# Performance work log

Hardware: AMD Instinct MI355X
Metric: run time of the kernel (lower is better)

The kernel has to match this reference:

```python
import jax, jax.numpy as jnp
import numpy as np

B, N, D_IN, D_OUT = 4, 2048, 1024, 1024


def setup_inputs() -> dict:
    key = jax.random.key(0)
    kx, kq, kk, kv = jax.random.split(key, 4)
    x = jax.random.normal(kx, (B, N, D_IN), dtype=jnp.float32)
    # torch Linear(d_in, d_out, bias=False): y = x @ W.T, W ~ U(-1/sqrt(d_in), 1/sqrt(d_in)).
    # Store as [d_in, d_out] so y = x @ W.
    bound = 1.0 / np.sqrt(D_IN)
    Wq = jax.random.uniform(kq, (D_IN, D_OUT), jnp.float32, -bound, bound)
    Wk = jax.random.uniform(kk, (D_IN, D_OUT), jnp.float32, -bound, bound)
    Wv = jax.random.uniform(kv, (D_IN, D_OUT), jnp.float32, -bound, bound)
    return {"x": x, "Wq": Wq, "Wk": Wk, "Wv": Wv}


def reference(x, Wq, Wk, Wv):
    # x: [B, N, d_in]
    q = jnp.einsum("bnd,de->bne", x, Wq)  # [B, N, d_out]
    k = jnp.einsum("bnd,de->bne", x, Wk)
    v = jnp.einsum("bnd,de->bne", x, Wv)
    n = x.shape[1]
    scores = jnp.einsum("bqe,bke->bqk", q, k)  # [B, N, N]
    causal = jnp.triu(jnp.ones((n, n), dtype=bool), k=1)  # True above diagonal -> masked
    scores = jnp.where(causal, -jnp.inf, scores)
    scale = 1.0 / jnp.sqrt(jnp.asarray(k.shape[-1], dtype=scores.dtype))
    weights = jax.nn.softmax(scores * scale, axis=-1)
    # dropout with drop_rate=0.0 is identity
    return jnp.einsum("bqk,bke->bqe", weights, v)  # [B, N, d_out]
```

## Files before the change

### kernel.cpp

```cpp
#include <hip/hip_runtime.h>

typedef float  f4v  __attribute__((ext_vector_type(4)));
typedef short  s8v  __attribute__((ext_vector_type(8)));

__device__ __forceinline__ ushort f2b(float f) {
    union { float f; unsigned int u; } v; v.f = f;
    unsigned int u = v.u;
    u += 0x7fffu + ((u >> 16) & 1u);
    return (ushort)(u >> 16);
}
__device__ __forceinline__ float b2f(ushort u) {
    union { unsigned int u; float f; } v; v.u = ((unsigned int)u) << 16;
    return v.f;
}

__device__ __forceinline__ void async16(const ushort* g, ushort* ldsp) {
    __builtin_amdgcn_global_load_lds(
        (const __attribute__((address_space(1))) unsigned int*)g,
        (__attribute__((address_space(3))) unsigned int*)ldsp, 16, 0, 0);
}

__global__ __launch_bounds__(256) void cast_f32_bf16(const float* __restrict__ in,
                                                     ushort* __restrict__ out,
                                                     float* __restrict__ l, int n4) {
    int i = blockIdx.x * 256 + threadIdx.x;
    if (i < 8192) l[i] = 0.f;
    if (i < n4) {
        float4 f = ((const float4*)in)[i];
        ushort4 o;
        o.x = f2b(f.x); o.y = f2b(f.y); o.z = f2b(f.z); o.w = f2b(f.w);
        ((ushort4*)out)[i] = o;
    }
}

__global__ __launch_bounds__(256) void transpose_cast(const float* __restrict__ w0,
                                                      const float* __restrict__ w1,
                                                      const float* __restrict__ w2,
                                                      ushort* __restrict__ out) {
    __shared__ float tile[32][33];
    const float* W = (blockIdx.z == 0) ? w0 : (blockIdx.z == 1 ? w1 : w2);
    ushort* O = out + (size_t)blockIdx.z * (1024u * 1024u);
    int x0 = blockIdx.x * 32, y0 = blockIdx.y * 32;
    int tx = threadIdx.x, ty = threadIdx.y;
    for (int i = 0; i < 4; i++)
        tile[ty + i * 8][tx] = W[(size_t)(y0 + ty + i * 8) * 1024 + x0 + tx];
    __syncthreads();
    for (int i = 0; i < 4; i++)
        O[(size_t)(x0 + ty + i * 8) * 1024 + y0 + tx] = f2b(tile[tx][ty + i * 8]);
}


#define RD_A4(buf_)                                                                   \
    _Pragma("unroll") for (int mi = 0; mi < 4; mi++)                                  \
    _Pragma("unroll") for (int s = 0; s < 2; s++)                                     \
        af[mi][s] = *(const s8v*)&(buf_)[(wm + mi * 16 + l16) * 64 +                  \
                                         (((s * 4 + quad) ^ (l16 & 7)) * 8)];

#define RD_B2(buf_, NI0_)                                                             \
    _Pragma("unroll") for (int j = 0; j < 2; j++)                                     \
    _Pragma("unroll") for (int s = 0; s < 2; s++)                                     \
        bf[j][s] = *(const s8v*)&(buf_)[(wn + ((NI0_) + j) * 16 + l16) * 64 +         \
                                        (((s * 4 + quad) ^ (l16 & 7)) * 8)];

#define MFMA16(NI0_)                                                                  \
    _Pragma("unroll") for (int mi = 0; mi < 4; mi++)                                  \
    _Pragma("unroll") for (int j = 0; j < 2; j++)                                     \
    _Pragma("unroll") for (int s = 0; s < 2; s++)                                     \
        acc[mi][(NI0_) + j] = __builtin_amdgcn_mfma_f32_16x16x32_bf16(                \
            af[mi][s], bf[j][s], acc[mi][(NI0_) + j], 0, 0, 0);

__global__ __launch_bounds__(512, 2) void gemm_qkv(const ushort* __restrict__ A,
                                                   const ushort* __restrict__ Wt,
                                                   ushort* __restrict__ q,
                                                   ushort* __restrict__ k,
                                                   ushort* __restrict__ vt) {
    constexpr int K = 1024;
    extern __shared__ ushort lds[];

    const int L = blockIdx.x;
    const int xcd = L & 7, idx = L >> 3;
    const int ci = xcd >> 1, cj = xcd & 1;
    const int mo = idx >> 3, no = idx & 7;
    const int m0 = (ci * 8 + mo) * 256;
    const int n0 = (cj * 8 + no) * 192;

    const int tid = threadIdx.x;
    const int w = tid >> 6, lane = tid & 63, quad = lane >> 4, l16 = lane & 15;
    const int wm = (w >> 1) * 64, wn = (w & 1) * 96;

    ushort* a0 = lds;
    ushort* a1 = lds + 16384;
    ushort* a2 = lds + 32768;
    ushort* b0 = lds + 49152;
    ushort* b1 = lds + 61440;

    const int lr = lane >> 3;
    const int lc8 = (lane & 7) ^ lr;
    const ushort* Ab = A  + (size_t)(m0 + w * 8 + lr) * K + lc8 * 8;
    const ushort* Bb = Wt + (size_t)(n0 + w * 8 + lr) * K + lc8 * 8;
    const int dW = w * 512;

#define ISSUE_A(buf_, kk_, a_) async16(Ab + (size_t)(a_) * 64 * K + (kk_), (buf_) + (a_) * 4096 + dW)
#define ISSUE_B(buf_, kk_, c_) async16(Bb + (size_t)(c_) * 64 * K + (kk_), (buf_) + (c_) * 4096 + dW)

    f4v acc[4][6];
    #pragma unroll
    for (int mi = 0; mi < 4; mi++)
        #pragma unroll
        for (int ni = 0; ni < 6; ni++) acc[mi][ni] = 0;

    #pragma unroll
    for (int a = 0; a < 4; a++) ISSUE_A(a0, 0, a);
    #pragma unroll
    for (int c = 0; c < 3; c++) ISSUE_B(b0, 0, c);
    #pragma unroll
    for (int a = 0; a < 4; a++) ISSUE_A(a1, 64, a);
    asm volatile("s_waitcnt vmcnt(4)" ::: "memory");
    asm volatile("s_barrier" ::: "memory");

    for (int t = 0; t < 16; ++t) {
        const int kB = (t + 1) * 64;
        const int kA = (t + 2) * 64;
        s8v af[4][2], bf[2][2];

        RD_A4(a0)
        RD_B2(b0, 0)
        if (t < 15) {
            ISSUE_B(b1, kB, 0);
            ISSUE_B(b1, kB, 1);
            ISSUE_B(b1, kB, 2);
        }
        asm volatile("s_barrier" ::: "memory");
        __builtin_amdgcn_s_setprio(1);
        MFMA16(0)
        __builtin_amdgcn_s_setprio(0);
        asm volatile("s_barrier" ::: "memory");

        RD_B2(b0, 2)
        if (t < 14) {
            ISSUE_A(a2, kA, 0);
            ISSUE_A(a2, kA, 1);
        }
        asm volatile("s_barrier" ::: "memory");
        __builtin_amdgcn_s_setprio(1);
        MFMA16(2)
        __builtin_amdgcn_s_setprio(0);
        asm volatile("s_barrier" ::: "memory");

        RD_B2(b0, 4)
        if (t < 14) {
            ISSUE_A(a2, kA, 2);
            ISSUE_A(a2, kA, 3);
        }
        asm volatile("s_barrier" ::: "memory");
        __builtin_amdgcn_s_setprio(1);
        MFMA16(4)
        __builtin_amdgcn_s_setprio(0);

        if (t < 14)       asm volatile("s_waitcnt vmcnt(4)" ::: "memory");
        else if (t == 14) asm volatile("s_waitcnt vmcnt(0)" ::: "memory");
        asm volatile("s_barrier" ::: "memory");

        ushort* ta = a0; a0 = a1; a1 = a2; a2 = ta;
        ushort* tb = b0; b0 = b1; b1 = tb;
    }

    #pragma unroll
    for (int mi = 0; mi < 4; mi++)
        #pragma unroll
        for (int ni = 0; ni < 6; ni++) {
            int row = m0 + wm + mi * 16 + quad * 4;
            int col = n0 + wn + ni * 16 + l16;
            int z = col >> 10, cz = col & 1023;
            f4v v = acc[mi][ni];
            if (z < 2) {
                ushort* C = (z == 0) ? q : k;
                #pragma unroll
                for (int rr = 0; rr < 4; rr++)
                    C[(size_t)(row + rr) * 1024 + cz] = f2b(v[rr]);
            } else {
                int b = row >> 11, tok = row & 2047;
                ushort4 pk;
                pk.x = f2b(v[0]); pk.y = f2b(v[1]); pk.z = f2b(v[2]); pk.w = f2b(v[3]);
                *(ushort4*)&vt[(size_t)b * (1024u * 2048u) + (size_t)cz * 2048 + tok] = pk;
            }
        }
#undef ISSUE_A
#undef ISSUE_B
}

__global__ __launch_bounds__(512, 2) void sgemm_qk(const ushort* __restrict__ Q,
                                                   const ushort* __restrict__ Km,
                                                   ushort* __restrict__ E,
                                                   float* __restrict__ l) {
    constexpr int K = 1024;
    extern __shared__ ushort lds[];

    const int L = blockIdx.x;
    const int xcd = L & 7, i = L >> 3;
    const int t = (xcd < 4) ? (xcd * 26 + i) : (104 + (xcd - 4) * 25 + i);
    const int b = t / 51;
    int tt = t - b * 51;
    int mt = 0;
    for (;; mt++) {
        int c = (4 * (mt + 1) + 2) / 3;
        if (tt < c) break;
        tt -= c;
    }
    const int nt = tt;
    const int m0 = mt * 256, n0 = nt * 192;
    const ushort* A  = Q  + (size_t)b * 2048 * 1024;
    const ushort* Bt = Km + (size_t)b * 2048 * 1024;
    ushort* Cb = E + (size_t)b * 2048 * 2048;
    float* lb = l + (size_t)b * 2048;

    const int tid = threadIdx.x;
    const int w = tid >> 6, lane = tid & 63, quad = lane >> 4, l16 = lane & 15;
    const int wm = (w >> 1) * 64, wn = (w & 1) * 96;

    ushort* a0 = lds;
    ushort* a1 = lds + 16384;
    ushort* a2 = lds + 32768;
    ushort* b0 = lds + 49152;
    ushort* b1 = lds + 61440;

    const int lr = lane >> 3;
    const int lc8 = (lane & 7) ^ lr;
    const ushort* Ab = A  + (size_t)(m0 + w * 8 + lr) * K + lc8 * 8;
    const ushort* Bb = Bt + (size_t)(n0 + w * 8 + lr) * K + lc8 * 8;
    const int dW = w * 512;

#define ISSUE_A(buf_, kk_, a_) async16(Ab + (size_t)(a_) * 64 * K + (kk_), (buf_) + (a_) * 4096 + dW)
#define ISSUE_B(buf_, kk_, c_) async16(Bb + (size_t)(c_) * 64 * K + (kk_), (buf_) + (c_) * 4096 + dW)

    f4v acc[4][6];
    #pragma unroll
    for (int mi = 0; mi < 4; mi++)
        #pragma unroll
        for (int ni = 0; ni < 6; ni++) acc[mi][ni] = 0;

    #pragma unroll
    for (int a = 0; a < 4; a++) ISSUE_A(a0, 0, a);
    #pragma unroll
    for (int c = 0; c < 3; c++) ISSUE_B(b0, 0, c);
    #pragma unroll
    for (int a = 0; a < 4; a++) ISSUE_A(a1, 64, a);
    asm volatile("s_waitcnt vmcnt(4)" ::: "memory");
    asm volatile("s_barrier" ::: "memory");

    for (int tk = 0; tk < 16; ++tk) {
        const int kB = (tk + 1) * 64;
        const int kA = (tk + 2) * 64;
        s8v af[4][2], bf[2][2];

        RD_A4(a0)
        RD_B2(b0, 0)
        if (tk < 15) {
            ISSUE_B(b1, kB, 0);
            ISSUE_B(b1, kB, 1);
            ISSUE_B(b1, kB, 2);
        }
        asm volatile("s_barrier" ::: "memory");
        __builtin_amdgcn_s_setprio(1);
        MFMA16(0)
        __builtin_amdgcn_s_setprio(0);
        asm volatile("s_barrier" ::: "memory");

        RD_B2(b0, 2)
        if (tk < 14) {
            ISSUE_A(a2, kA, 0);
            ISSUE_A(a2, kA, 1);
        }
        asm volatile("s_barrier" ::: "memory");
        __builtin_amdgcn_s_setprio(1);
        MFMA16(2)
        __builtin_amdgcn_s_setprio(0);
        asm volatile("s_barrier" ::: "memory");

        RD_B2(b0, 4)
        if (tk < 14) {
            ISSUE_A(a2, kA, 2);
            ISSUE_A(a2, kA, 3);
        }
        asm volatile("s_barrier" ::: "memory");
        __builtin_amdgcn_s_setprio(1);
        MFMA16(4)
        __builtin_amdgcn_s_setprio(0);

        if (tk < 14)       asm volatile("s_waitcnt vmcnt(4)" ::: "memory");
        else if (tk == 14) asm volatile("s_waitcnt vmcnt(0)" ::: "memory");
        asm volatile("s_barrier" ::: "memory");

        ushort* ta = a0; a0 = a1; a1 = a2; a2 = ta;
        ushort* tb = b0; b0 = b1; b1 = tb;
    }

    #pragma unroll
    for (int mi = 0; mi < 4; mi++) {
        float rs[4] = {0.f, 0.f, 0.f, 0.f};
        #pragma unroll
        for (int ni = 0; ni < 6; ni++) {
            const int colbase = n0 + wn + ni * 16;
            if (colbase >= 2048) continue;
            const int col = colbase + l16;
            f4v v = acc[mi][ni];
            #pragma unroll
            for (int rr = 0; rr < 4; rr++) {
                const int row = m0 + wm + mi * 16 + quad * 4 + rr;
                float e = (col <= row) ? __expf(v[rr] * 0.03125f) : 0.f;
                ushort eb = f2b(e);
                Cb[(size_t)row * 2048 + col] = eb;
                rs[rr] += b2f(eb);
            }
        }
        #pragma unroll
        for (int rr = 0; rr < 4; rr++) {
            float s = rs[rr];
            s += __shfl_xor(s, 1);
            s += __shfl_xor(s, 2);
            s += __shfl_xor(s, 4);
            s += __shfl_xor(s, 8);
            if (l16 == 0)
                atomicAdd(&lb[m0 + wm + mi * 16 + quad * 4 + rr], s);
        }
    }
#undef ISSUE_A
#undef ISSUE_B
}

__global__ __launch_bounds__(512, 2) void gemm_pv(const ushort* __restrict__ Em,
                                                  const ushort* __restrict__ Vt,
                                                  const float* __restrict__ l,
                                                  float* __restrict__ Out) {
    extern __shared__ ushort lds[];
    const int L = blockIdx.x;
    const int t = (L & 7) * 32 + (L >> 3);
    const int b = t >> 6;
    const int mt = (t >> 3) & 7;
    const int nt = t & 7;
    const int m0 = mt * 256, n0 = nt * 128;
    const int NT = 4 * (mt + 1);
    const ushort* A  = Em + (size_t)b * 2048 * 2048;
    const ushort* Bt = Vt + (size_t)b * 1024 * 2048;
    const float* lb = l + (size_t)b * 2048;
    float* C = Out + (size_t)b * 2048 * 1024;

    const int tid = threadIdx.x;
    const int w = tid >> 6, lane = tid & 63, quad = lane >> 4, l16 = lane & 15;
    const int wm = (w >> 1) * 64, wn = (w & 1) * 64;

    ushort* a0 = lds;
    ushort* a1 = lds + 16384;
    ushort* a2 = lds + 32768;
    ushort* b0 = lds + 49152;
    ushort* b1 = lds + 57344;

    const int lr = lane >> 3;
    const int lc8 = (lane & 7) ^ lr;
    const ushort* Ab = A  + (size_t)(m0 + w * 8 + lr) * 2048 + lc8 * 8;
    const ushort* Bb = Bt + (size_t)(n0 + w * 8 + lr) * 2048 + lc8 * 8;
    const int dW = w * 512;

#define ISSUE_A(buf_, kk_, a_) async16(Ab + (size_t)(a_) * 64 * 2048 + (kk_), (buf_) + (a_) * 4096 + dW)
#define ISSUE_B(buf_, kk_, c_) async16(Bb + (size_t)(c_) * 64 * 2048 + (kk_), (buf_) + (c_) * 4096 + dW)

    f4v acc[4][4];
    #pragma unroll
    for (int mi = 0; mi < 4; mi++)
        #pragma unroll
        for (int ni = 0; ni < 4; ni++) acc[mi][ni] = 0;

    #pragma unroll
    for (int a = 0; a < 4; a++) ISSUE_A(a0, 0, a);
    #pragma unroll
    for (int c = 0; c < 2; c++) ISSUE_B(b0, 0, c);
    #pragma unroll
    for (int a = 0; a < 4; a++) ISSUE_A(a1, 64, a);
    asm volatile("s_waitcnt vmcnt(4)" ::: "memory");
    asm volatile("s_barrier" ::: "memory");

    for (int tk = 0; tk < NT; ++tk) {
        const int kB = (tk + 1) * 64;
        const int kA = (tk + 2) * 64;
        s8v af[4][2], bf[2][2];

        RD_A4(a0)
        RD_B2(b0, 0)
        if (tk < NT - 1) {
            ISSUE_B(b1, kB, 0);
            ISSUE_B(b1, kB, 1);
        }
        if (tk < NT - 2) {
            ISSUE_A(a2, kA, 0);
            ISSUE_A(a2, kA, 1);
        }
        asm volatile("s_barrier" ::: "memory");
        __builtin_amdgcn_s_setprio(1);
        MFMA16(0)
        __builtin_amdgcn_s_setprio(0);
        asm volatile("s_barrier" ::: "memory");

        RD_B2(b0, 2)
        if (tk < NT - 2) {
            ISSUE_A(a2, kA, 2);
            ISSUE_A(a2, kA, 3);
        }
        asm volatile("s_barrier" ::: "memory");
        __builtin_amdgcn_s_setprio(1);
        MFMA16(2)
        __builtin_amdgcn_s_setprio(0);

        if (tk < NT - 2)       asm volatile("s_waitcnt vmcnt(4)" ::: "memory");
        else if (tk == NT - 2) asm volatile("s_waitcnt vmcnt(0)" ::: "memory");
        asm volatile("s_barrier" ::: "memory");

        ushort* ta = a0; a0 = a1; a1 = a2; a2 = ta;
        ushort* tb = b0; b0 = b1; b1 = tb;
    }

    #pragma unroll
    for (int mi = 0; mi < 4; mi++) {
        const int row = m0 + wm + mi * 16 + quad * 4;
        float inv[4];
        #pragma unroll
        for (int rr = 0; rr < 4; rr++) inv[rr] = 1.f / lb[row + rr];
        #pragma unroll
        for (int ni = 0; ni < 4; ni++) {
            const int col = n0 + wn + ni * 16 + l16;
            f4v v = acc[mi][ni];
            #pragma unroll
            for (int rr = 0; rr < 4; rr++)
                C[(size_t)(row + rr) * 1024 + col] = v[rr] * inv[rr];
        }
    }
#undef ISSUE_A
#undef ISSUE_B
}

extern "C" void kernel_launch(void* const* d_in, const int* in_sizes, int n_in,
                              void* d_out, int out_size, void* d_ws, size_t ws_size,
                              hipStream_t stream) {
    const float* x  = (const float*)d_in[0];
    const float* Wq = (const float*)d_in[1];
    const float* Wk = (const float*)d_in[2];
    const float* Wv = (const float*)d_in[3];
    float* out = (float*)d_out;

    static bool init = false;
    if (!init) {
        hipFuncSetAttribute(reinterpret_cast<const void*>(gemm_qkv),
                            hipFuncAttributeMaxDynamicSharedMemorySize, 147456);
        hipFuncSetAttribute(reinterpret_cast<const void*>(sgemm_qk),
                            hipFuncAttributeMaxDynamicSharedMemorySize, 147456);
        hipFuncSetAttribute(reinterpret_cast<const void*>(gemm_pv),
                            hipFuncAttributeMaxDynamicSharedMemorySize, 131072);
        init = true;
    }

    char* ws = (char*)d_ws;
    const size_t MiB = 1u << 20;
    ushort* xb = (ushort*)(ws);
    ushort* wt = (ushort*)(ws + 16 * MiB);
    ushort* q  = (ushort*)(ws + 22 * MiB);
    ushort* k  = (ushort*)(ws + 38 * MiB);
    ushort* vt = (ushort*)(ws + 54 * MiB);
    ushort* E  = (ushort*)(ws + 70 * MiB);
    float*  l  = (float*)(ws + 102 * MiB);

    cast_f32_bf16<<<(8192 * 1024 / 4) / 256, 256, 0, stream>>>(x, xb, l, 8192 * 1024 / 4);
    transpose_cast<<<dim3(32, 32, 3), dim3(32, 8), 0, stream>>>(Wq, Wk, Wv, wt);

    gemm_qkv<<<512, 512, 147456, stream>>>(xb, wt, q, k, vt);
    sgemm_qk<<<204, 512, 147456, stream>>>(q, k, E, l);
    gemm_pv<<<256, 512, 131072, stream>>>(E, vt, l, out);
}
```

Baseline: 213.5 us.

## Split PV GEMM over K into two halves with atomic output accumulation

Doubles the PV grid by splitting each causal tile's K range into two halves, ordering blocks so the longest tiles launch first, and accumulating partial results into the output with float atomics. The output buffer is zeroed inside the cast kernel. This targets load imbalance and low occupancy from the triangular work distribution, at the cost of atomic traffic, an extra full-size zero write, and non-deterministic summation order.

Result: slower. 249.0 us (+16.6%).

```diff
diff --git a/kernel.cpp b/kernel.cpp
--- a/kernel.cpp
+++ b/kernel.cpp
@@ -22,7 +22,8 @@
 
 __global__ __launch_bounds__(256) void cast_f32_bf16(const float* __restrict__ in,
                                                      ushort* __restrict__ out,
-                                                     float* __restrict__ l, int n4) {
+                                                     float* __restrict__ l,
+                                                     float* __restrict__ oz, int n4) {
     int i = blockIdx.x * 256 + threadIdx.x;
     if (i < 8192) l[i] = 0.f;
     if (i < n4) {
@@ -30,6 +31,8 @@
         ushort4 o;
         o.x = f2b(f.x); o.y = f2b(f.y); o.z = f2b(f.z); o.w = f2b(f.w);
         ((ushort4*)out)[i] = o;
+        float4 z; z.x = 0.f; z.y = 0.f; z.z = 0.f; z.w = 0.f;
+        ((float4*)oz)[i] = z;
     }
 }
 
@@ -333,13 +336,16 @@
                                                   const float* __restrict__ l,
                                                   float* __restrict__ Out) {
     extern __shared__ ushort lds[];
-    const int L = blockIdx.x;
-    const int t = (L & 7) * 32 + (L >> 3);
-    const int b = t >> 6;
-    const int mt = (t >> 3) & 7;
-    const int nt = t & 7;
+    const int p = blockIdx.x;
+    const int g = p >> 6;
+    const int r = p & 63;
+    const int b = r >> 4;
+    const int h = (r >> 3) & 1;
+    const int nt = r & 7;
+    const int mt = 7 - g;
+    const int NTh = 2 * (mt + 1);
+    const int K0 = h * NTh * 64;
     const int m0 = mt * 256, n0 = nt * 128;
-    const int NT = 4 * (mt + 1);
     const ushort* A  = Em + (size_t)b * 2048 * 2048;
     const ushort* Bt = Vt + (size_t)b * 1024 * 2048;
     const float* lb = l + (size_t)b * 2048;
@@ -357,8 +363,8 @@
 
     const int lr = lane >> 3;
     const int lc8 = (lane & 7) ^ lr;
-    const ushort* Ab = A  + (size_t)(m0 + w * 8 + lr) * 2048 + lc8 * 8;
-    const ushort* Bb = Bt + (size_t)(n0 + w * 8 + lr) * 2048 + lc8 * 8;
+    const ushort* Ab = A  + (size_t)(m0 + w * 8 + lr) * 2048 + K0 + lc8 * 8;
+    const ushort* Bb = Bt + (size_t)(n0 + w * 8 + lr) * 2048 + K0 + lc8 * 8;
     const int dW = w * 512;
 
 #define ISSUE_A(buf_, kk_, a_) async16(Ab + (size_t)(a_) * 64 * 2048 + (kk_), (buf_) + (a_) * 4096 + dW)
@@ -379,18 +385,18 @@
     asm volatile("s_waitcnt vmcnt(4)" ::: "memory");
     asm volatile("s_barrier" ::: "memory");
 
-    for (int tk = 0; tk < NT; ++tk) {
+    for (int tk = 0; tk < NTh; ++tk) {
         const int kB = (tk + 1) * 64;
         const int kA = (tk + 2) * 64;
         s8v af[4][2], bf[2][2];
 
         RD_A4(a0)
         RD_B2(b0, 0)
-        if (tk < NT - 1) {
+        if (tk < NTh - 1) {
             ISSUE_B(b1, kB, 0);
             ISSUE_B(b1, kB, 1);
         }
-        if (tk < NT - 2) {
+        if (tk < NTh - 2) {
             ISSUE_A(a2, kA, 0);
             ISSUE_A(a2, kA, 1);
         }
@@ -401,7 +407,7 @@
         asm volatile("s_barrier" ::: "memory");
 
         RD_B2(b0, 2)
-        if (tk < NT - 2) {
+        if (tk < NTh - 2) {
             ISSUE_A(a2, kA, 2);
             ISSUE_A(a2, kA, 3);
         }
@@ -410,8 +416,8 @@
         MFMA16(2)
         __builtin_amdgcn_s_setprio(0);
 
-        if (tk < NT - 2)       asm volatile("s_waitcnt vmcnt(4)" ::: "memory");
-        else if (tk == NT - 2) asm volatile("s_waitcnt vmcnt(0)" ::: "memory");
+        if (tk < NTh - 2)       asm volatile("s_waitcnt vmcnt(4)" ::: "memory");
+        else if (tk == NTh - 2) asm volatile("s_waitcnt vmcnt(0)" ::: "memory");
         asm volatile("s_barrier" ::: "memory");
 
         ushort* ta = a0; a0 = a1; a1 = a2; a2 = ta;
@@ -430,7 +436,7 @@
             f4v v = acc[mi][ni];
             #pragma unroll
             for (int rr = 0; rr < 4; rr++)
-                C[(size_t)(row + rr) * 1024 + col] = v[rr] * inv[rr];
+                atomicAdd(&C[(size_t)(row + rr) * 1024 + col], v[rr] * inv[rr]);
         }
     }
 #undef ISSUE_A
@@ -467,10 +473,10 @@
     ushort* E  = (ushort*)(ws + 70 * MiB);
     float*  l  = (float*)(ws + 102 * MiB);
 
-    cast_f32_bf16<<<(8192 * 1024 / 4) / 256, 256, 0, stream>>>(x, xb, l, 8192 * 1024 / 4);
+    cast_f32_bf16<<<(8192 * 1024 / 4) / 256, 256, 0, stream>>>(x, xb, l, out, 8192 * 1024 / 4);
     transpose_cast<<<dim3(32, 32, 3), dim3(32, 8), 0, stream>>>(Wq, Wk, Wv, wt);
 
     gemm_qkv<<<512, 512, 147456, stream>>>(xb, wt, q, k, vt);
     sgemm_qk<<<204, 512, 147456, stream>>>(q, k, E, l);
-    gemm_pv<<<256, 512, 131072, stream>>>(E, vt, l, out);
-}
+    gemm_pv<<<512, 512, 131072, stream>>>(E, vt, l, out);
+}
```
